# Kernel optimization log

Hardware: AMD Instinct MI355X
Metric: run time of the kernel (lower is better)

## Reference

```python
import jax, jax.numpy as jnp
import numpy as np

B, S, H = 32, 1024, 512  # batch, src_len, hidden_dim


def setup_inputs() -> dict:
    key = jax.random.key(0)
    k1, k2, k3, k4, k5 = jax.random.split(key, 5)
    hidden = jax.random.normal(k1, (B, H), dtype=jnp.float32)
    encoder_outputs = jax.random.normal(k2, (B, S, 2 * H), dtype=jnp.float32)
    # nn.Linear(3H, H): weight stored here as [3H, H] (input-major) with bias [H]
    W = jax.random.normal(k3, (3 * H, H), dtype=jnp.float32) / np.sqrt(3 * H)
    b = jax.random.normal(k4, (H,), dtype=jnp.float32) * 0.01
    v = jax.random.normal(k5, (H,), dtype=jnp.float32) / np.sqrt(H)
    return {"hidden": hidden, "encoder_outputs": encoder_outputs, "W": W, "b": b, "v": v}


def reference(hidden, encoder_outputs, W, b, v):
    # concat((repeat(hidden), encoder_outputs)) @ W  ==  hidden @ W[:H] (broadcast) + enc @ W[H:]
    Wh, We = W[:H], W[H:]                         # [H,H], [2H,H]
    h_proj = hidden @ Wh                           # [B,H]
    e_proj = jnp.einsum('bse,eh->bsh', encoder_outputs, We)  # [B,S,H]
    energy = jnp.tanh(h_proj[:, None, :] + e_proj + b)       # [B,S,H]
    # bmm(v[B,1,H], energy^T[B,H,S]) -> scores [B,S]
    scores = jnp.einsum('bsh,h->bs', energy, v)
    return jax.nn.softmax(scores, axis=1)
```

## Files before the change

kernel.cpp:

```cpp
#include <hip/hip_runtime.h>
#include <math.h>

#define B_ 32
#define S_ 1024
#define H_ 512
#define K_ 1024
#define M_ (B_ * S_)

typedef __attribute__((ext_vector_type(8))) short bf16x8;
typedef __attribute__((ext_vector_type(4))) float f32x4;

__device__ __forceinline__ void split_bf16(float f, unsigned short& hi, unsigned short& lo) {
    unsigned u = __float_as_uint(f);
    unsigned rh = (u + 0x7fffu + ((u >> 16) & 1u)) >> 16;
    hi = (unsigned short)rh;
    float fh = __uint_as_float(rh << 16);
    float r = f - fh;
    unsigned ur = __float_as_uint(r);
    unsigned rl = (ur + 0x7fffu + ((ur >> 16) & 1u)) >> 16;
    lo = (unsigned short)rl;
}

__device__ __forceinline__ void split8_store(const float4& x, const float4& y,
                                             unsigned short* hiP, unsigned short* loP) {
    union { unsigned short us[8]; uint4 u; } h, l;
    split_bf16(x.x, h.us[0], l.us[0]);
    split_bf16(x.y, h.us[1], l.us[1]);
    split_bf16(x.z, h.us[2], l.us[2]);
    split_bf16(x.w, h.us[3], l.us[3]);
    split_bf16(y.x, h.us[4], l.us[4]);
    split_bf16(y.y, h.us[5], l.us[5]);
    split_bf16(y.z, h.us[6], l.us[6]);
    split_bf16(y.w, h.us[7], l.us[7]);
    *reinterpret_cast<uint4*>(hiP) = h.u;
    *reinterpret_cast<uint4*>(loP) = l.u;
}

__device__ __forceinline__ void async_copy16(const void* g, void* l) {
    __builtin_amdgcn_global_load_lds(
        (const __attribute__((address_space(1))) void*)g,
        (__attribute__((address_space(3))) void*)l, 16, 0, 0);
}

__global__ __launch_bounds__(256) void prep_kernel(
    const float* __restrict__ hidden, const float* __restrict__ W,
    const float* __restrict__ bias, float* __restrict__ hb,
    unsigned short* __restrict__ Wh, unsigned short* __restrict__ Wl)
{
    __shared__ float red[4][64];
    __shared__ float t[32][33];
    const int bx = blockIdx.x;
    if (bx < 256) {
        const int tid = threadIdx.x;
        const int h0  = (bx & 7) * 64;
        const int b   = bx >> 3;
        const int h   = h0 + (tid & 63);
        const int ks  = tid >> 6;
        const float* hrow = hidden + b * H_;
        float acc = 0.f;
        #pragma unroll 8
        for (int k = ks * 128; k < ks * 128 + 128; ++k)
            acc = fmaf(hrow[k], W[(size_t)k * H_ + h], acc);
        red[ks][tid & 63] = acc;
        __syncthreads();
        if (tid < 64)
            hb[b * H_ + h0 + tid] = red[0][tid] + red[1][tid] + red[2][tid]
                                  + red[3][tid] + bias[h0 + tid];
    } else {
        const float* We = W + (size_t)H_ * H_;
        const int cx = bx - 256;
        const int k0 = (cx & 31) * 32, n0 = (cx >> 5) * 32;
        const int tx = threadIdx.x & 31, ty = threadIdx.x >> 5;
        #pragma unroll
        for (int j = 0; j < 4; ++j) {
            const int k = ty + 8 * j;
            t[k][tx] = We[(size_t)(k0 + k) * H_ + n0 + tx];
        }
        __syncthreads();
        #pragma unroll
        for (int j = 0; j < 4; ++j) {
            const int n = ty + 8 * j;
            unsigned short hi, lo;
            split_bf16(t[tx][n], hi, lo);
            Wh[(size_t)(n0 + n) * K_ + k0 + tx] = hi;
            Wl[(size_t)(n0 + n) * K_ + k0 + tx] = lo;
        }
    }
}

__global__ __launch_bounds__(256, 2) void gemm_fused(
    const float* __restrict__ EO,
    const unsigned short* __restrict__ Bth,
    const unsigned short* __restrict__ Btl,
    const float* __restrict__ hb, const float* __restrict__ v,
    float* __restrict__ partial)
{
    __shared__ unsigned short ldsA[2][2][4096];
    __shared__ unsigned short ldsB[2][2][4096];

    const int tid  = threadIdx.x;
    const int nt   = blockIdx.x;
    const int mt   = blockIdx.y;
    const int row0 = mt * 128;
    const int col0 = nt * 128;
    const int batch = row0 >> 10;

    const int lane   = tid & 63;
    const int wave   = tid >> 6;
    const int wm     = wave >> 1, wn = wave & 1;
    const int lanelo = lane & 15, quad = lane >> 4;

    size_t gaA[2];
    int offA[2];
    #pragma unroll
    for (int s = 0; s < 2; ++s) {
        const int seg = tid + 256 * s;
        const int m = seg >> 2, sg = seg & 3;
        gaA[s] = (size_t)(row0 + m) * K_ + sg * 8;
        offA[s] = m * 32 + (sg ^ ((m >> 1) & 3)) * 8;
    }
    size_t gb[2];
    int offB[2];
    #pragma unroll
    for (int j = 0; j < 2; ++j) {
        const int iss = wave * 2 + j;
        const int r   = iss * 16 + (lane >> 2);
        const int qg  = (lane & 3) ^ ((r >> 1) & 3);
        gb[j] = (size_t)(col0 + r) * K_ + qg * 8;
        offB[j] = iss * 512;
    }

    f32x4 acc[4][4];
    #pragma unroll
    for (int i = 0; i < 4; ++i)
        #pragma unroll
        for (int j = 0; j < 4; ++j)
            acc[i][j] = (f32x4){0.f, 0.f, 0.f, 0.f};

    float4 a0[2], a1[2];
    #pragma unroll
    for (int s = 0; s < 2; ++s) {
        a0[s] = *reinterpret_cast<const float4*>(EO + gaA[s]);
        a1[s] = *reinterpret_cast<const float4*>(EO + gaA[s] + 4);
    }
    #pragma unroll
    for (int j = 0; j < 2; ++j) {
        async_copy16(Bth + gb[j], &ldsB[0][0][offB[j]]);
        async_copy16(Btl + gb[j], &ldsB[0][1][offB[j]]);
    }
    #pragma unroll
    for (int s = 0; s < 2; ++s)
        split8_store(a0[s], a1[s], &ldsA[0][0][offA[s]], &ldsA[0][1][offA[s]]);

    for (int i = 0; i < 32; ++i) {
        __syncthreads();
        const int cur = i & 1, nxt = cur ^ 1;
        const int k0n = 32 * (i + 1);
        if (i < 31) {
            #pragma unroll
            for (int s = 0; s < 2; ++s) {
                a0[s] = *reinterpret_cast<const float4*>(EO + gaA[s] + k0n);
                a1[s] = *reinterpret_cast<const float4*>(EO + gaA[s] + k0n + 4);
            }
            #pragma unroll
            for (int j = 0; j < 2; ++j) {
                async_copy16(Bth + gb[j] + k0n, &ldsB[nxt][0][offB[j]]);
                async_copy16(Btl + gb[j] + k0n, &ldsB[nxt][1][offB[j]]);
            }
        }

        bf16x8 a_h[4], a_l[4], b_h[4], b_l[4];
        #pragma unroll
        for (int fi = 0; fi < 4; ++fi) {
            const int m  = wm * 64 + fi * 16 + lanelo;
            const int sa = quad ^ ((m >> 1) & 3);
            a_h[fi] = *reinterpret_cast<const bf16x8*>(&ldsA[cur][0][m * 32 + sa * 8]);
            a_l[fi] = *reinterpret_cast<const bf16x8*>(&ldsA[cur][1][m * 32 + sa * 8]);
            const int n  = wn * 64 + fi * 16 + lanelo;
            const int sb = quad ^ ((n >> 1) & 3);
            b_h[fi] = *reinterpret_cast<const bf16x8*>(&ldsB[cur][0][n * 32 + sb * 8]);
            b_l[fi] = *reinterpret_cast<const bf16x8*>(&ldsB[cur][1][n * 32 + sb * 8]);
        }
        #pragma unroll
        for (int fi = 0; fi < 4; ++fi)
            #pragma unroll
            for (int fj = 0; fj < 4; ++fj) {
                acc[fi][fj] = __builtin_amdgcn_mfma_f32_16x16x32_bf16(
                    a_h[fi], b_h[fj], acc[fi][fj], 0, 0, 0);
                acc[fi][fj] = __builtin_amdgcn_mfma_f32_16x16x32_bf16(
                    a_h[fi], b_l[fj], acc[fi][fj], 0, 0, 0);
                acc[fi][fj] = __builtin_amdgcn_mfma_f32_16x16x32_bf16(
                    a_l[fi], b_h[fj], acc[fi][fj], 0, 0, 0);
            }

        if (i < 31) {
            #pragma unroll
            for (int s = 0; s < 2; ++s)
                split8_store(a0[s], a1[s],
                             &ldsA[nxt][0][offA[s]], &ldsA[nxt][1][offA[s]]);
        }
    }

    const float* hb_row = hb + batch * H_;
    float hbv[4], vv[4];
    #pragma unroll
    for (int fj = 0; fj < 4; ++fj) {
        const int c = col0 + wn * 64 + fj * 16 + lanelo;
        hbv[fj] = hb_row[c];
        vv[fj]  = v[c];
    }
    float* red = reinterpret_cast<float*>(&ldsA[0][0][0]);
    #pragma unroll
    for (int fi = 0; fi < 4; ++fi)
        #pragma unroll
        for (int r = 0; r < 4; ++r) {
            float rs = 0.f;
            #pragma unroll
            for (int fj = 0; fj < 4; ++fj)
                rs = fmaf(tanhf(acc[fi][fj][r] + hbv[fj]), vv[fj], rs);
            rs += __shfl_xor(rs, 1, 64);
            rs += __shfl_xor(rs, 2, 64);
            rs += __shfl_xor(rs, 4, 64);
            rs += __shfl_xor(rs, 8, 64);
            if (lanelo == 0) {
                const int row = wm * 64 + fi * 16 + quad * 4 + r;
                red[row * 2 + wn] = rs;
            }
        }
    __syncthreads();
    if (tid < 128)
        partial[(size_t)nt * M_ + row0 + tid] = red[tid * 2] + red[tid * 2 + 1];
}

__global__ __launch_bounds__(256) void softmax_kernel(
    const float* __restrict__ partial, float* __restrict__ out)
{
    const int b = blockIdx.x;
    const int tid = threadIdx.x;
    float val[4];
    float lmax = -3.0e38f;
    #pragma unroll
    for (int q = 0; q < 4; ++q) {
        const int idx = b * S_ + tid + 256 * q;
        float sum = partial[idx] + partial[M_ + idx] + partial[2 * M_ + idx] +
                    partial[3 * M_ + idx];
        val[q] = sum;
        lmax = fmaxf(lmax, sum);
    }
    #pragma unroll
    for (int off = 32; off > 0; off >>= 1)
        lmax = fmaxf(lmax, __shfl_down(lmax, off, 64));
    __shared__ float wmax[4];
    if ((tid & 63) == 0) wmax[tid >> 6] = lmax;
    __syncthreads();
    const float gmax = fmaxf(fmaxf(wmax[0], wmax[1]), fmaxf(wmax[2], wmax[3]));
    float lsum = 0.0f;
    #pragma unroll
    for (int q = 0; q < 4; ++q) {
        val[q] = expf(val[q] - gmax);
        lsum += val[q];
    }
    #pragma unroll
    for (int off = 32; off > 0; off >>= 1)
        lsum += __shfl_down(lsum, off, 64);
    __shared__ float wsum[4];
    if ((tid & 63) == 0) wsum[tid >> 6] = lsum;
    __syncthreads();
    const float inv = 1.0f / (wsum[0] + wsum[1] + wsum[2] + wsum[3]);
    #pragma unroll
    for (int q = 0; q < 4; ++q)
        out[b * S_ + tid + 256 * q] = val[q] * inv;
}

extern "C" void kernel_launch(void* const* d_in, const int* in_sizes, int n_in,
                              void* d_out, int out_size, void* d_ws, size_t ws_size,
                              hipStream_t stream) {
    const float* hidden = (const float*)d_in[0];
    const float* EO     = (const float*)d_in[1];
    const float* W      = (const float*)d_in[2];
    const float* bias   = (const float*)d_in[3];
    const float* v      = (const float*)d_in[4];
    float* out          = (float*)d_out;

    float* hb      = (float*)d_ws;
    float* partial = hb + B_ * H_;
    unsigned short* Wth = (unsigned short*)(partial + 4 * M_);
    unsigned short* Wtl = Wth + (size_t)H_ * K_;

    prep_kernel<<<768, 256, 0, stream>>>(hidden, W, bias, hb, Wth, Wtl);
    gemm_fused<<<dim3(4, M_ / 128), 256, 0, stream>>>(EO, Wth, Wtl, hb, v, partial);
    softmax_kernel<<<B_, 256, 0, stream>>>(partial, out);
}
```

Measured before the change: 317.0 us.

## Load A fragments directly from global into registers, drop A LDS staging

The GEMM no longer stages the fp32 encoder tile through LDS. Each lane loads its own A fragment from global memory and splits it into bf16 hi/lo with truncation instead of round-to-nearest. This halves LDS use, which allows raising the occupancy hint to 3 blocks per CU, and it remaps block ids so 8 M-tiles share each N-tile group for L2 reuse. The prep kernel is also split into two kernels. The costs are redundant global loads of A across the two wn waves, slightly lower split precision, and one extra launch.

```diff
diff --git a/kernel.cpp b/kernel.cpp
--- a/kernel.cpp
+++ b/kernel.cpp
@@ -21,19 +21,19 @@
     lo = (unsigned short)rl;
 }
 
-__device__ __forceinline__ void split8_store(const float4& x, const float4& y,
-                                             unsigned short* hiP, unsigned short* loP) {
-    union { unsigned short us[8]; uint4 u; } h, l;
-    split_bf16(x.x, h.us[0], l.us[0]);
-    split_bf16(x.y, h.us[1], l.us[1]);
-    split_bf16(x.z, h.us[2], l.us[2]);
-    split_bf16(x.w, h.us[3], l.us[3]);
-    split_bf16(y.x, h.us[4], l.us[4]);
-    split_bf16(y.y, h.us[5], l.us[5]);
-    split_bf16(y.z, h.us[6], l.us[6]);
-    split_bf16(y.w, h.us[7], l.us[7]);
-    *reinterpret_cast<uint4*>(hiP) = h.u;
-    *reinterpret_cast<uint4*>(loP) = l.u;
+__device__ __forceinline__ void cheap_split8(const float4& x, const float4& y,
+                                             bf16x8& h, bf16x8& l) {
+    union { unsigned short us[8]; bf16x8 v; } H, L;
+    const float f[8] = {x.x, x.y, x.z, x.w, y.x, y.y, y.z, y.w};
+    #pragma unroll
+    for (int j = 0; j < 8; ++j) {
+        const unsigned u = __float_as_uint(f[j]);
+        H.us[j] = (unsigned short)(u >> 16);
+        const float r = f[j] - __uint_as_float(u & 0xffff0000u);
+        L.us[j] = (unsigned short)(__float_as_uint(r) >> 16);
+    }
+    h = H.v;
+    l = L.v;
 }
 
 __device__ __forceinline__ void async_copy16(const void* g, void* l) {
@@ -42,65 +42,64 @@
         (__attribute__((address_space(3))) void*)l, 16, 0, 0);
 }
 
-__global__ __launch_bounds__(256) void prep_kernel(
+__global__ __launch_bounds__(256) void hproj_kernel(
     const float* __restrict__ hidden, const float* __restrict__ W,
-    const float* __restrict__ bias, float* __restrict__ hb,
-    unsigned short* __restrict__ Wh, unsigned short* __restrict__ Wl)
-{
+    const float* __restrict__ bias, float* __restrict__ hb)
+{
+    const int tid = threadIdx.x;
+    const int h0  = blockIdx.x * 64;
+    const int b   = blockIdx.y;
+    const int h   = h0 + (tid & 63);
+    const int ks  = tid >> 6;
+    const float* hrow = hidden + b * H_;
+    float acc = 0.f;
+    #pragma unroll 8
+    for (int k = ks * 128; k < ks * 128 + 128; ++k)
+        acc = fmaf(hrow[k], W[(size_t)k * H_ + h], acc);
     __shared__ float red[4][64];
+    red[ks][tid & 63] = acc;
+    __syncthreads();
+    if (tid < 64)
+        hb[b * H_ + h0 + tid] = red[0][tid] + red[1][tid] + red[2][tid]
+                              + red[3][tid] + bias[h0 + tid];
+}
+
+__global__ __launch_bounds__(256) void conv_we_kernel(
+    const float* __restrict__ We, unsigned short* __restrict__ Wh,
+    unsigned short* __restrict__ Wl)
+{
     __shared__ float t[32][33];
-    const int bx = blockIdx.x;
-    if (bx < 256) {
-        const int tid = threadIdx.x;
-        const int h0  = (bx & 7) * 64;
-        const int b   = bx >> 3;
-        const int h   = h0 + (tid & 63);
-        const int ks  = tid >> 6;
-        const float* hrow = hidden + b * H_;
-        float acc = 0.f;
-        #pragma unroll 8
-        for (int k = ks * 128; k < ks * 128 + 128; ++k)
-            acc = fmaf(hrow[k], W[(size_t)k * H_ + h], acc);
-        red[ks][tid & 63] = acc;
-        __syncthreads();
-        if (tid < 64)
-            hb[b * H_ + h0 + tid] = red[0][tid] + red[1][tid] + red[2][tid]
-                                  + red[3][tid] + bias[h0 + tid];
-    } else {
-        const float* We = W + (size_t)H_ * H_;
-        const int cx = bx - 256;
-        const int k0 = (cx & 31) * 32, n0 = (cx >> 5) * 32;
-        const int tx = threadIdx.x & 31, ty = threadIdx.x >> 5;
-        #pragma unroll
-        for (int j = 0; j < 4; ++j) {
-            const int k = ty + 8 * j;
-            t[k][tx] = We[(size_t)(k0 + k) * H_ + n0 + tx];
-        }
-        __syncthreads();
-        #pragma unroll
-        for (int j = 0; j < 4; ++j) {
-            const int n = ty + 8 * j;
-            unsigned short hi, lo;
-            split_bf16(t[tx][n], hi, lo);
-            Wh[(size_t)(n0 + n) * K_ + k0 + tx] = hi;
-            Wl[(size_t)(n0 + n) * K_ + k0 + tx] = lo;
-        }
-    }
-}
-
-__global__ __launch_bounds__(256, 2) void gemm_fused(
+    const int tx = threadIdx.x & 31, ty = threadIdx.x >> 5;
+    const int k0 = blockIdx.x * 32, n0 = blockIdx.y * 32;
+    #pragma unroll
+    for (int j = 0; j < 4; ++j) {
+        const int k = ty + 8 * j;
+        t[k][tx] = We[(size_t)(k0 + k) * H_ + n0 + tx];
+    }
+    __syncthreads();
+    #pragma unroll
+    for (int j = 0; j < 4; ++j) {
+        const int n = ty + 8 * j;
+        unsigned short hi, lo;
+        split_bf16(t[tx][n], hi, lo);
+        Wh[(size_t)(n0 + n) * K_ + k0 + tx] = hi;
+        Wl[(size_t)(n0 + n) * K_ + k0 + tx] = lo;
+    }
+}
+
+__global__ __launch_bounds__(256, 3) void gemm_fused(
     const float* __restrict__ EO,
     const unsigned short* __restrict__ Bth,
     const unsigned short* __restrict__ Btl,
     const float* __restrict__ hb, const float* __restrict__ v,
     float* __restrict__ partial)
 {
-    __shared__ unsigned short ldsA[2][2][4096];
     __shared__ unsigned short ldsB[2][2][4096];
 
-    const int tid  = threadIdx.x;
-    const int nt   = blockIdx.x;
-    const int mt   = blockIdx.y;
+    const int tid = threadIdx.x;
+    const int bid = blockIdx.x;
+    const int mt = (bid & 7) + ((bid >> 5) << 3);
+    const int nt = (bid >> 3) & 3;
     const int row0 = mt * 128;
     const int col0 = nt * 128;
     const int batch = row0 >> 10;
@@ -110,15 +109,6 @@
     const int wm     = wave >> 1, wn = wave & 1;
     const int lanelo = lane & 15, quad = lane >> 4;
 
-    size_t gaA[2];
-    int offA[2];
-    #pragma unroll
-    for (int s = 0; s < 2; ++s) {
-        const int seg = tid + 256 * s;
-        const int m = seg >> 2, sg = seg & 3;
-        gaA[s] = (size_t)(row0 + m) * K_ + sg * 8;
-        offA[s] = m * 32 + (sg ^ ((m >> 1) & 3)) * 8;
-    }
     size_t gb[2];
     int offB[2];
     #pragma unroll
@@ -130,6 +120,9 @@
         offB[j] = iss * 512;
     }
 
+    const float* aptr = EO + (size_t)(row0 + wm * 64 + lanelo) * K_ + quad * 8;
+    const int AFI = 16 * K_;
+
     f32x4 acc[4][4];
     #pragma unroll
     for (int i = 0; i < 4; ++i)
@@ -137,20 +130,17 @@
         for (int j = 0; j < 4; ++j)
             acc[i][j] = (f32x4){0.f, 0.f, 0.f, 0.f};
 
-    float4 a0[2], a1[2];
-    #pragma unroll
-    for (int s = 0; s < 2; ++s) {
-        a0[s] = *reinterpret_cast<const float4*>(EO + gaA[s]);
-        a1[s] = *reinterpret_cast<const float4*>(EO + gaA[s] + 4);
-    }
     #pragma unroll
     for (int j = 0; j < 2; ++j) {
         async_copy16(Bth + gb[j], &ldsB[0][0][offB[j]]);
         async_copy16(Btl + gb[j], &ldsB[0][1][offB[j]]);
     }
-    #pragma unroll
-    for (int s = 0; s < 2; ++s)
-        split8_store(a0[s], a1[s], &ldsA[0][0][offA[s]], &ldsA[0][1][offA[s]]);
+    float4 af0[4], af1[4];
+    #pragma unroll
+    for (int fi = 0; fi < 4; ++fi) {
+        af0[fi] = *reinterpret_cast<const float4*>(aptr + fi * AFI);
+        af1[fi] = *reinterpret_cast<const float4*>(aptr + fi * AFI + 4);
+    }
 
     for (int i = 0; i < 32; ++i) {
         __syncthreads();
@@ -158,46 +148,38 @@
         const int k0n = 32 * (i + 1);
         if (i < 31) {
             #pragma unroll
-            for (int s = 0; s < 2; ++s) {
-                a0[s] = *reinterpret_cast<const float4*>(EO + gaA[s] + k0n);
-                a1[s] = *reinterpret_cast<const float4*>(EO + gaA[s] + k0n + 4);
-            }
-            #pragma unroll
             for (int j = 0; j < 2; ++j) {
                 async_copy16(Bth + gb[j] + k0n, &ldsB[nxt][0][offB[j]]);
                 async_copy16(Btl + gb[j] + k0n, &ldsB[nxt][1][offB[j]]);
             }
         }
 
-        bf16x8 a_h[4], a_l[4], b_h[4], b_l[4];
+        bf16x8 b_h[4], b_l[4];
+        #pragma unroll
+        for (int fj = 0; fj < 4; ++fj) {
+            const int n  = wn * 64 + fj * 16 + lanelo;
+            const int sb = quad ^ ((n >> 1) & 3);
+            b_h[fj] = *reinterpret_cast<const bf16x8*>(&ldsB[cur][0][n * 32 + sb * 8]);
+            b_l[fj] = *reinterpret_cast<const bf16x8*>(&ldsB[cur][1][n * 32 + sb * 8]);
+        }
+
         #pragma unroll
         for (int fi = 0; fi < 4; ++fi) {
-            const int m  = wm * 64 + fi * 16 + lanelo;
-            const int sa = quad ^ ((m >> 1) & 3);
-            a_h[fi] = *reinterpret_cast<const bf16x8*>(&ldsA[cur][0][m * 32 + sa * 8]);
-            a_l[fi] = *reinterpret_cast<const bf16x8*>(&ldsA[cur][1][m * 32 + sa * 8]);
-            const int n  = wn * 64 + fi * 16 + lanelo;
-            const int sb = quad ^ ((n >> 1) & 3);
-            b_h[fi] = *reinterpret_cast<const bf16x8*>(&ldsB[cur][0][n * 32 + sb * 8]);
-            b_l[fi] = *reinterpret_cast<const bf16x8*>(&ldsB[cur][1][n * 32 + sb * 8]);
-        }
-        #pragma unroll
-        for (int fi = 0; fi < 4; ++fi)
+            bf16x8 ah, al;
+            cheap_split8(af0[fi], af1[fi], ah, al);
+            if (i < 31) {
+                af0[fi] = *reinterpret_cast<const float4*>(aptr + fi * AFI + k0n);
+                af1[fi] = *reinterpret_cast<const float4*>(aptr + fi * AFI + k0n + 4);
+            }
             #pragma unroll
             for (int fj = 0; fj < 4; ++fj) {
                 acc[fi][fj] = __builtin_amdgcn_mfma_f32_16x16x32_bf16(
-                    a_h[fi], b_h[fj], acc[fi][fj], 0, 0, 0);
+                    ah, b_h[fj], acc[fi][fj], 0, 0, 0);
                 acc[fi][fj] = __builtin_amdgcn_mfma_f32_16x16x32_bf16(
-                    a_h[fi], b_l[fj], acc[fi][fj], 0, 0, 0);
+                    ah, b_l[fj], acc[fi][fj], 0, 0, 0);
                 acc[fi][fj] = __builtin_amdgcn_mfma_f32_16x16x32_bf16(
-                    a_l[fi], b_h[fj], acc[fi][fj], 0, 0, 0);
-            }
-
-        if (i < 31) {
-            #pragma unroll
-            for (int s = 0; s < 2; ++s)
-                split8_store(a0[s], a1[s],
-                             &ldsA[nxt][0][offA[s]], &ldsA[nxt][1][offA[s]]);
+                    al, b_h[fj], acc[fi][fj], 0, 0, 0);
+            }
         }
     }
 
@@ -209,7 +191,7 @@
         hbv[fj] = hb_row[c];
         vv[fj]  = v[c];
     }
-    float* red = reinterpret_cast<float*>(&ldsA[0][0][0]);
+    float* red = reinterpret_cast<float*>(&ldsB[0][0][0]);
     #pragma unroll
     for (int fi = 0; fi < 4; ++fi)
         #pragma unroll
@@ -287,7 +269,10 @@
     unsigned short* Wth = (unsigned short*)(partial + 4 * M_);
     unsigned short* Wtl = Wth + (size_t)H_ * K_;
 
-    prep_kernel<<<768, 256, 0, stream>>>(hidden, W, bias, hb, Wth, Wtl);
-    gemm_fused<<<dim3(4, M_ / 128), 256, 0, stream>>>(EO, Wth, Wtl, hb, v, partial);
+    const float* We = W + (size_t)H_ * H_;
+
+    hproj_kernel<<<dim3(8, B_), 256, 0, stream>>>(hidden, W, bias, hb);
+    conv_we_kernel<<<dim3(K_ / 32, H_ / 32), 256, 0, stream>>>(We, Wth, Wtl);
+    gemm_fused<<<1024, 256, 0, stream>>>(EO, Wth, Wtl, hb, v, partial);
     softmax_kernel<<<B_, 256, 0, stream>>>(partial, out);
 }
```

Measured after the change: 396.7 us. 1.25x slower.
